# Optimization experiments

Hardware: AMD Instinct MI355X
Metric: run time of the kernel (lower is better)

## Reference

```python
import jax, jax.numpy as jnp
import numpy as np
import math

KV_STRIDE = 2
Q_STRIDE = 1
WAVE_LEN = 1000.0
POS_MAG = 1.0


def _pos_embed(h, w, h_kv, w_kv, q_stride, kv_stride, feat_dim):
    # Sinusoidal relative-position embeddings, matching get_position_embedding.
    h_idx = jnp.arange(h, dtype=jnp.float32) * q_stride
    w_idx = jnp.arange(w, dtype=jnp.float32) * q_stride
    h_kv_idx = jnp.arange(h_kv, dtype=jnp.float32) * kv_stride
    w_kv_idx = jnp.arange(w_kv, dtype=jnp.float32) * kv_stride
    h_diff = (h_idx[:, None] - h_kv_idx[None, :]) * POS_MAG  # (h, h_kv)
    w_diff = (w_idx[:, None] - w_kv_idx[None, :]) * POS_MAG  # (w, w_kv)
    feat_range = jnp.arange(feat_dim // 4, dtype=jnp.float32)
    dim_mat = WAVE_LEN ** (4.0 / feat_dim * feat_range)  # (feat_dim//4,)
    wd = w_diff[:, :, None] / dim_mat  # (w, w_kv, F)
    hd = h_diff[:, :, None] / dim_mat  # (h, h_kv, F)
    emb_x = jnp.concatenate([jnp.sin(wd), jnp.cos(wd)], axis=2)  # (w, w_kv, feat_dim//2)
    emb_y = jnp.concatenate([jnp.sin(hd), jnp.cos(hd)], axis=2)  # (h, h_kv, feat_dim//2)
    return emb_x, emb_y


def setup_inputs() -> dict:
    key = jax.random.key(0)
    ks = jax.random.split(key, 11)
    C = 288
    s = 1.0 / math.sqrt(C)
    return {
        'x_input': jax.random.normal(ks[0], (2, C, 64, 64), jnp.float32),
        'Wq': jax.random.normal(ks[1], (C, C), jnp.float32) * s,
        'Wk': jax.random.normal(ks[2], (C, C), jnp.float32) * s,
        'Wv': jax.random.normal(ks[3], (C, C), jnp.float32) * s,
        'Wx': jax.random.normal(ks[4], (C, C // 2), jnp.float32) * s,
        'Wy': jax.random.normal(ks[5], (C, C // 2), jnp.float32) * s,
        'Wproj': jax.random.normal(ks[6], (C, C), jnp.float32) * s,
        'bproj': jax.random.normal(ks[7], (C,), jnp.float32) * 0.02,
        'Wc': jax.random.normal(ks[8], (9, C), jnp.float32) * s,
        'bc': jax.random.normal(ks[9], (9,), jnp.float32) * 0.02,
        'gamma': jax.random.normal(ks[10], (1,), jnp.float32),
    }


def reference(x_input, Wq, Wk, Wv, Wx, Wy, Wproj, bproj, Wc, bc, gamma):
    M = Wc.shape[0]                       # num_mixtures
    n, C, h, w = x_input.shape
    d = Wq.shape[0] // M                  # qk_embed_dim (== v_dim)
    x_q = x_input                         # q_stride == 1
    x_kv = x_input[:, :, ::KV_STRIDE, ::KV_STRIDE]  # AvgPool2d(k=1, stride=2)
    h_kv, w_kv = x_kv.shape[2], x_kv.shape[3]

    # 1x1 convs as channel GEMMs
    q = jnp.einsum('nchw,oc->nohw', x_q, Wq).reshape(n, M, d, h * w)
    q = q.transpose(0, 1, 3, 2)                                    # (n,M,hw,d)
    k = jnp.einsum('nchw,oc->nohw', x_kv, Wk).reshape(n, M, d, h_kv * w_kv)

    emb_x, emb_y = _pos_embed(h, w, h_kv, w_kv, Q_STRIDE, KV_STRIDE, C)
    inv_sqrt2 = 1.0 / math.sqrt(2.0)
    pf_x = (emb_x @ Wx.T).reshape(w, w_kv, M, d).transpose(2, 0, 1, 3) * inv_sqrt2  # (M,w,w_kv,d)
    pf_y = (emb_y @ Wy.T).reshape(h, h_kv, M, d).transpose(2, 0, 1, 3) * inv_sqrt2  # (M,h,h_kv,d)

    energy = jnp.matmul(q, k).reshape(n, M, h, w, h_kv, w_kv)
    q5 = q.reshape(n, M, h, w, d)
    e_x = jnp.einsum('nmhwd,mwvd->nmhwv', q5, pf_x)  # (n,M,h,w,w_kv)
    e_y = jnp.einsum('nmhwd,mhud->nmhwu', q5, pf_y)  # (n,M,h,w,h_kv)
    energy = energy + e_x[:, :, :, :, None, :] + e_y[:, :, :, :, :, None]
    energy = energy.reshape(n, M, h * w, h_kv * w_kv)
    attn = jax.nn.softmax(energy, axis=3)

    # Learned per-mixture gating from mean query context
    context = q.transpose(0, 1, 3, 2).reshape(n, M * d, h * w).mean(axis=2)  # (n, M*d)
    mix_w = jax.nn.softmax(context @ Wc.T + bc, axis=1)                      # (n, M)
    attn = jnp.sum(attn * mix_w[:, :, None, None], axis=1)                   # (n,hw,hw_kv)

    v = jnp.einsum('nchw,oc->nohw', x_kv, Wv).reshape(n, M * d, h_kv * w_kv)
    v = v.transpose(0, 2, 1)                                                 # (n,hw_kv,M*d)
    out = jnp.matmul(attn, v).transpose(0, 2, 1).reshape(n, M * d, h, w)
    out = jnp.einsum('nchw,oc->nohw', out, Wproj) + bproj[None, :, None, None]
    return gamma[0] * out + x_input
```

## Files before the change

kernel.cpp:

```cpp
#include <hip/hip_runtime.h>
#include <math.h>

#define NB     2
#define CDIM   288
#define HW     4096
#define PKV    1024
#define MHEAD  9
#define DHEAD  32

typedef __attribute__((ext_vector_type(8))) short bf16x8;
typedef __attribute__((ext_vector_type(4))) float f32x4;

#if __has_builtin(__builtin_amdgcn_exp2f)
#define EXP2(x) __builtin_amdgcn_exp2f(x)
#else
#define EXP2(x) exp2f(x)
#endif

__device__ inline unsigned short f2bf(float x) {
    unsigned int u = __float_as_uint(x);
    u = (u + 0x7fffu + ((u >> 16) & 1u)) >> 16;
    return (unsigned short)u;
}


__global__ __launch_bounds__(256) void prep(const float* __restrict__ X,
        const float* __restrict__ Wq, const float* __restrict__ Wk,
        const float* __restrict__ Wv, const float* __restrict__ Wproj,
        const float* __restrict__ Wx, const float* __restrict__ Wy,
        unsigned short* __restrict__ XF, unsigned short* __restrict__ WFq,
        unsigned short* __restrict__ WFk, unsigned short* __restrict__ WFv,
        unsigned short* __restrict__ WFp, float* __restrict__ WTx,
        float* __restrict__ WTy, float* __restrict__ MX) {
    __shared__ float t32[32][133];
    __shared__ float t16[16][17];
    __shared__ float red[4];
    int b = blockIdx.x;
    int tid = threadIdx.x;
    if (b < 576) {
        int bx = b % 32, by = (b / 32) % 9, n = b / 288;
        int j0 = bx * 128, c0 = by * 32;
        int c = tid >> 3, f = tid & 7;
        const float* src = &X[((size_t)n * CDIM + c0 + c) * HW + j0];
#pragma unroll
        for (int l = 0; l < 4; ++l) {
            float4 v = *(const float4*)&src[(f + l * 8) * 4];
            *(float4*)&t32[c][(f + l * 8) * 4] = v;
        }
        __syncthreads();
        int cc = c0 >> 5;
#pragma unroll
        for (int l = 0; l < 4; ++l) {
            int g = l * 256 + tid;
            int s = g >> 7;
            int w = g & 127;
            int lane = w >> 1, e0 = (w & 1) * 4;
            int jl = s * 16 + (lane & 15);
            int cb = (lane >> 4) * 8 + e0;
            unsigned int w0 = f2bf(t32[cb + 0][jl]) | ((unsigned int)f2bf(t32[cb + 1][jl]) << 16);
            unsigned int w1 = f2bf(t32[cb + 2][jl]) | ((unsigned int)f2bf(t32[cb + 3][jl]) << 16);
            int jt = (j0 >> 4) + s;
            unsigned short* O = XF + (size_t)n * HW * CDIM + ((size_t)jt * 9 + cc) * 512 + lane * 8 + e0;
            uint2 pk = { w0, w1 };
            *(uint2*)O = pk;
        }
    } else if (b < 900) {
        int u = b - 576;
        int bx = u % 9, by = (u / 9) % 18, bz = u / 162;
        const float* W = bz ? Wy : Wx;
        float* WT      = bz ? WTy : WTx;
        int f0 = bx * 16, o0 = by * 16;
        int tx = tid & 15, ty = tid >> 4;
        t16[ty][tx] = W[(o0 + ty) * 144 + f0 + tx];
        __syncthreads();
        WT[(f0 + ty) * 288 + o0 + tx] = t16[tx][ty];
    } else if (b < 1062) {
        int t = b - 900;
        int sub = tid >> 6, lane = tid & 63;
        int ot = t / 9, cc = t % 9;
        const float* W = (sub == 0) ? Wq : (sub == 1) ? Wk : (sub == 2) ? Wv : Wproj;
        unsigned short* O = ((sub == 0) ? WFq : (sub == 1) ? WFk : (sub == 2) ? WFv : WFp)
                            + (size_t)t * 512;
        int o  = ot * 16 + (lane & 15);
        int c0 = cc * 32 + (lane >> 4) * 8;
        const float* src = W + (size_t)o * CDIM + c0;
        float4 f0 = *(const float4*)src, f1 = *(const float4*)(src + 4);
        unsigned int v0 = f2bf(f0.x) | ((unsigned int)f2bf(f0.y) << 16);
        unsigned int v1 = f2bf(f0.z) | ((unsigned int)f2bf(f0.w) << 16);
        unsigned int v2 = f2bf(f1.x) | ((unsigned int)f2bf(f1.y) << 16);
        unsigned int v3 = f2bf(f1.z) | ((unsigned int)f2bf(f1.w) << 16);
        uint4 pk = { v0, v1, v2, v3 };
        *(uint4*)(O + lane * 8) = pk;
    } else {
        int bid = b - 1062;
        const float* xr = X + (size_t)bid * HW;
        float s = 0.f;
        for (int j = tid; j < HW; j += 256) s += xr[j];
        for (int off = 32; off > 0; off >>= 1) s += __shfl_xor(s, off, 64);
        if ((tid & 63) == 0) red[tid >> 6] = s;
        __syncthreads();
        if (tid == 0) MX[bid] = (red[0] + red[1] + red[2] + red[3]) * (1.f / 4096.f);
    }
}

__global__ __launch_bounds__(256) void mid(
        const float* __restrict__ WTx, const float* __restrict__ WTy,
        unsigned short* __restrict__ FXb, unsigned short* __restrict__ FYb,
        const float* __restrict__ Wq, const float* __restrict__ MX,
        const float* __restrict__ Wc, const float* __restrict__ bc,
        float* __restrict__ MIXW,
        const unsigned short* __restrict__ WFq, const unsigned short* __restrict__ WFk,
        const unsigned short* __restrict__ WFv, const unsigned short* __restrict__ XF,
        unsigned short* __restrict__ Qf, unsigned short* __restrict__ KF,
        unsigned short* __restrict__ VF) {
    __shared__ float emb[144];
    __shared__ float ctx_s[NB * CDIM];
    __shared__ float lg[18];
    __shared__ __attribute__((aligned(16))) unsigned short tr[4][32][40];
    int b = blockIdx.x;
    int tid = threadIdx.x;

    if (b < 252) {
        int axis = b / 126;
        int dif  = b % 126;
        float diff = (float)(dif - 62);
        if (tid < 72) {
            float dm = expf(6.9077552789821368f * ((float)tid * (1.f / 72.f)));
            float t  = diff / dm;
            emb[tid]      = sinf(t);
            emb[72 + tid] = cosf(t);
        }
        __syncthreads();
        const float* WT = axis ? WTy : WTx;
        unsigned short* F = axis ? FYb : FXb;
        for (int o = tid; o < CDIM; o += 256) {
            float s = 0.f;
#pragma unroll 8
            for (int f = 0; f < 144; ++f) s += emb[f] * WT[f * 288 + o];
            int m = o >> 5, d = o & 31;
            F[(size_t)(m * 8 + (dif >> 4)) * 512 + ((dif & 15) + 16 * (d >> 3)) * 8 + (d & 7)]
                = f2bf(s * 0.70710678118654752f);
        }
    } else if (b == 252) {
        for (int idx = tid; idx < 1152; idx += 256) {
            int d = idx & 31, rr = (idx >> 5) & 1, mm = (idx >> 6) % 9, ax = idx / 576;
            int dif = 126 + rr;
            unsigned short* F = ax ? FYb : FXb;
            F[(size_t)(mm * 8 + 7) * 512 + ((dif & 15) + 16 * (d >> 3)) * 8 + (d & 7)] = 0;
        }
        for (int p = tid; p < NB * CDIM; p += 256) {
            int n = p / CDIM, o = p % CDIM;
            const float* wr = Wq + (size_t)o * CDIM;
            const float* mx = MX + n * CDIM;
            float s = 0.f;
            for (int c = 0; c < CDIM; c += 4) {
                float4 w4 = *(const float4*)&wr[c];
                float4 m4 = *(const float4*)&mx[c];
                s += w4.x * m4.x + w4.y * m4.y + w4.z * m4.z + w4.w * m4.w;
            }
            ctx_s[p] = s;
        }
        __syncthreads();
        if (tid < 18) {
            int n = tid / 9, j = tid % 9;
            float s = bc[j];
            for (int o = 0; o < CDIM; ++o) s += ctx_s[n * CDIM + o] * Wc[j * CDIM + o];
            lg[tid] = s;
        }
        __syncthreads();
        if (tid < 2) {
            float mx = -1e30f;
            for (int j = 0; j < 9; ++j) mx = fmaxf(mx, lg[tid * 9 + j]);
            float e[9], sm = 0.f;
            for (int j = 0; j < 9; ++j) { e[j] = __expf(lg[tid * 9 + j] - mx); sm += e[j]; }
            for (int j = 0; j < 9; ++j) MIXW[tid * 9 + j] = e[j] / sm;
        }
    } else {
        int bx = b - 253;
        int gx = bx % 40;
        int m  = (bx / 40) % 9;
        int n  = bx / 360;
        int wv = tid >> 6, lane = tid & 63;
        int lq = lane & 15, quad = lane >> 4;
        if (gx < 32) {
            int j0 = gx * 128;
            int jw = j0 + wv * 32;
            const unsigned short* Wb = WFq + ((size_t)(m * 2) * 9) * 512 + lane * 8;
            const unsigned short* Xb = XF + (size_t)n * HW * CDIM + ((size_t)(jw >> 4) * 9) * 512 + lane * 8;
            f32x4 acc[2][2] = {};
#pragma unroll
            for (int cc = 0; cc < 9; ++cc) {
                bf16x8 a0 = *(const bf16x8*)(Wb + (size_t)cc * 512);
                bf16x8 a1 = *(const bf16x8*)(Wb + (size_t)(9 + cc) * 512);
                bf16x8 b0 = *(const bf16x8*)(Xb + (size_t)cc * 512);
                bf16x8 b1 = *(const bf16x8*)(Xb + (size_t)(9 + cc) * 512);
                acc[0][0] = __builtin_amdgcn_mfma_f32_16x16x32_bf16(a0, b0, acc[0][0], 0, 0, 0);
                acc[0][1] = __builtin_amdgcn_mfma_f32_16x16x32_bf16(a0, b1, acc[0][1], 0, 0, 0);
                acc[1][0] = __builtin_amdgcn_mfma_f32_16x16x32_bf16(a1, b0, acc[1][0], 0, 0, 0);
                acc[1][1] = __builtin_amdgcn_mfma_f32_16x16x32_bf16(a1, b1, acc[1][1], 0, 0, 0);
            }
#pragma unroll
            for (int oi = 0; oi < 2; ++oi)
#pragma unroll
                for (int ji = 0; ji < 2; ++ji)
#pragma unroll
                    for (int r = 0; r < 4; ++r)
                        tr[wv][ji * 16 + lq][oi * 16 + quad * 4 + r]
                            = f2bf(1.4426950408889634f * acc[oi][ji][r]);
            int jl = lane & 31, half = lane >> 5;
            bf16x8 v0 = *(const bf16x8*)&tr[wv][jl][half * 16];
            bf16x8 v1 = *(const bf16x8*)&tr[wv][jl][half * 16 + 8];
            unsigned short* Qm = Qf + ((size_t)(n * MHEAD + m) * HW + jw + jl) * 32 + half * 16;
            *(bf16x8*)Qm = v0;
            *(bf16x8*)(Qm + 8) = v1;
        } else {
            int p0 = (gx - 32) * 128;
            int pw = p0 + wv * 32;
            const unsigned short* XFn = XF + (size_t)n * HW * CDIM;
            size_t bidx[2];
#pragma unroll
            for (int pi = 0; pi < 2; ++pi) {
                int p   = pw + pi * 16 + lq;
                int pos = ((p >> 5) << 7) + ((p & 31) << 1);
                bidx[pi] = ((size_t)(pos >> 4) * 9) * 512 + ((pos & 15) + 16 * quad) * 8;
            }
            const unsigned short* Wkb = WFk + ((size_t)(m * 2) * 9) * 512 + lane * 8;
            const unsigned short* Wvb = WFv + ((size_t)(m * 2) * 9) * 512 + lane * 8;
            f32x4 ak[2][2] = {}, av[2][2] = {};
#pragma unroll
            for (int cc = 0; cc < 9; ++cc) {
                bf16x8 a0k = *(const bf16x8*)(Wkb + (size_t)cc * 512);
                bf16x8 a1k = *(const bf16x8*)(Wkb + (size_t)(9 + cc) * 512);
                bf16x8 a0v = *(const bf16x8*)(Wvb + (size_t)cc * 512);
                bf16x8 a1v = *(const bf16x8*)(Wvb + (size_t)(9 + cc) * 512);
                bf16x8 b0  = *(const bf16x8*)(XFn + bidx[0] + (size_t)cc * 512);
                bf16x8 b1  = *(const bf16x8*)(XFn + bidx[1] + (size_t)cc * 512);
                ak[0][0] = __builtin_amdgcn_mfma_f32_16x16x32_bf16(a0k, b0, ak[0][0], 0, 0, 0);
                ak[0][1] = __builtin_amdgcn_mfma_f32_16x16x32_bf16(a0k, b1, ak[0][1], 0, 0, 0);
                ak[1][0] = __builtin_amdgcn_mfma_f32_16x16x32_bf16(a1k, b0, ak[1][0], 0, 0, 0);
                ak[1][1] = __builtin_amdgcn_mfma_f32_16x16x32_bf16(a1k, b1, ak[1][1], 0, 0, 0);
                av[0][0] = __builtin_amdgcn_mfma_f32_16x16x32_bf16(a0v, b0, av[0][0], 0, 0, 0);
                av[0][1] = __builtin_amdgcn_mfma_f32_16x16x32_bf16(a0v, b1, av[0][1], 0, 0, 0);
                av[1][0] = __builtin_amdgcn_mfma_f32_16x16x32_bf16(a1v, b0, av[1][0], 0, 0, 0);
                av[1][1] = __builtin_amdgcn_mfma_f32_16x16x32_bf16(a1v, b1, av[1][1], 0, 0, 0);
            }
#pragma unroll
            for (int oi = 0; oi < 2; ++oi)
#pragma unroll
                for (int pi = 0; pi < 2; ++pi)
#pragma unroll
                    for (int r = 0; r < 4; ++r)
                        tr[wv][pi * 16 + lq][oi * 16 + quad * 4 + r] = f2bf(ak[oi][pi][r]);
            unsigned short* KFm = KF + (size_t)(n * MHEAD + m) * (PKV * 32);
#pragma unroll
            for (int pi = 0; pi < 2; ++pi) {
                bf16x8 v = *(const bf16x8*)&tr[wv][pi * 16 + lq][quad * 8];
                *(bf16x8*)(KFm + (size_t)((pw >> 4) + pi) * 512 + lane * 8) = v;
            }
#pragma unroll
            for (int oi = 0; oi < 2; ++oi)
#pragma unroll
                for (int pi = 0; pi < 2; ++pi)
#pragma unroll
                    for (int r = 0; r < 4; ++r)
                        tr[wv][oi * 16 + quad * 4 + r][pi * 16 + lq] = f2bf(av[oi][pi][r]);
            unsigned short* VFn = VF + (size_t)n * CDIM * PKV;
#pragma unroll
            for (int oi = 0; oi < 2; ++oi) {
                bf16x8 v = *(const bf16x8*)&tr[wv][oi * 16 + lq][quad * 8];
                *(bf16x8*)(VFn + (size_t)((m * 2 + oi) * 32 + (pw >> 5)) * 512 + lane * 8) = v;
            }
        }
    }
}

__global__ __launch_bounds__(1024, 4) void attn_fused7(
        const unsigned short* __restrict__ Qf, const unsigned short* __restrict__ KF,
        const unsigned short* __restrict__ VF, const unsigned short* __restrict__ WFp,
        const unsigned short* __restrict__ FXb, const unsigned short* __restrict__ FYb,
        const float* __restrict__ MIXW, const float* __restrict__ bproj,
        const float* __restrict__ x, const float* __restrict__ gamma,
        float* __restrict__ OUT) {
    int n    = blockIdx.x >> 7;
    int i0   = (blockIdx.x & 127) * 32;
    int tid  = threadIdx.x;
    int wv   = tid >> 6;
    int ti   = wv >> 3;
    int w8   = wv & 7;
    int lane = tid & 63;
    int lq   = lane & 15;
    int quad = lane >> 4;
    int it0  = i0 + ti * 16;

    int bx_t = (it0 & 63) >> 4;
    int hh   = i0 >> 6;
    int by_t = hh >> 4;
    int dh   = hh & 15;

    __shared__ __attribute__((aligned(16))) unsigned short tr[32][1032];
    float (*Rx_s)[2][16][82] = reinterpret_cast<float (*)[2][16][82]>((char*)&tr[0][0]);
    float (*Ry_s)[2][16][82] = reinterpret_cast<float (*)[2][16][82]>((char*)&tr[0][0] + 20992);
    float (*ws_s)[2][16][8]  = reinterpret_cast<float (*)[2][16][8]>((char*)&tr[0][0] + 41984);
    unsigned short (*Mt)[296] = reinterpret_cast<unsigned short (*)[296]>(&tr[0][0]);

    float mixed[8][4];
#pragma unroll
    for (int t = 0; t < 8; ++t)
#pragma unroll
        for (int j = 0; j < 4; ++j) mixed[t][j] = 0.f;

    auto r_phase = [&](int mm, bf16x8 af) {
        int pp = mm & 1;
        if (w8 < 5) {
            bf16x8 bR = *(const bf16x8*)(FXb + (size_t)(mm * 8 + bx_t + w8) * 512 + lane * 8);
            f32x4 r = (f32x4){0.f, 0.f, 0.f, 0.f};
            r = __builtin_amdgcn_mfma_f32_16x16x32_bf16(af, bR, r, 0, 0, 0);
#pragma unroll
            for (int reg = 0; reg < 4; ++reg)
                Rx_s[pp][ti][quad * 4 + reg][w8 * 16 + lq] = r[reg];
        } else {
            bf16x8 bR = *(const bf16x8*)(FYb + (size_t)(mm * 8 + by_t + (w8 - 5)) * 512 + lane * 8);
            f32x4 r = (f32x4){0.f, 0.f, 0.f, 0.f};
            r = __builtin_amdgcn_mfma_f32_16x16x32_bf16(af, bR, r, 0, 0, 0);
#pragma unroll
            for (int reg = 0; reg < 4; ++reg)
                Ry_s[pp][ti][quad * 4 + reg][(w8 - 5) * 16 + lq] = r[reg];
        }
        if (w8 < 2) {
            bf16x8 bR = *(const bf16x8*)(FYb + (size_t)(mm * 8 + by_t + 3 + w8) * 512 + lane * 8);
            f32x4 r = (f32x4){0.f, 0.f, 0.f, 0.f};
            r = __builtin_amdgcn_mfma_f32_16x16x32_bf16(af, bR, r, 0, 0, 0);
#pragma unroll
            for (int reg = 0; reg < 4; ++reg)
                Ry_s[pp][ti][quad * 4 + reg][(3 + w8) * 16 + lq] = r[reg];
        }
    };

    bf16x8 af_cur = *(const bf16x8*)(Qf + (((size_t)n * MHEAD) * HW + it0 + lq) * 32 + quad * 8);
    r_phase(0, af_cur);
    __syncthreads();

#pragma unroll 1
    for (int m = 0; m < MHEAD; ++m) {
        const unsigned short* KmF = KF + (size_t)(n * MHEAD + m) * (PKV * 32);
        bf16x8 kf[8];
#pragma unroll
        for (int t = 0; t < 8; ++t)
            kf[t] = *(const bf16x8*)(KmF + (size_t)(w8 * 8 + t) * 512 + lane * 8);

        bf16x8 af_nxt = af_cur;
        __builtin_amdgcn_s_setprio(1);
        if (m + 1 < MHEAD) {
            af_nxt = *(const bf16x8*)(Qf + (((size_t)(n * MHEAD + m + 1)) * HW + it0 + lq) * 32 + quad * 8);
            r_phase(m + 1, af_nxt);
        }
        f32x4 acc[8];
#pragma unroll
        for (int t = 0; t < 8; ++t) {
            f32x4 z = (f32x4){0.f, 0.f, 0.f, 0.f};
            acc[t] = __builtin_amdgcn_mfma_f32_16x16x32_bf16(af_cur, kf[t], z, 0, 0, 0);
        }
        __builtin_amdgcn_s_setprio(0);

        int par = m & 1;
        float exA[4], exB[4];
#pragma unroll
        for (int j = 0; j < 4; ++j) {
            int q = quad * 4 + j;
            exA[j] = Rx_s[par][ti][q][q + 62 - 2 * lq];
            exB[j] = Rx_s[par][ti][q][q + 30 - 2 * lq];
        }
        float rs[4] = {0.f, 0.f, 0.f, 0.f};
#pragma unroll
        for (int tp = 0; tp < 4; ++tp) {
            int u = w8 * 4 + tp;
            float ey[4];
#pragma unroll
            for (int j = 0; j < 4; ++j) ey[j] = Ry_s[par][ti][quad * 4 + j][dh + 62 - 2 * u];
#pragma unroll
            for (int half = 0; half < 2; ++half) {
                int t = tp * 2 + half;
#pragma unroll
                for (int j = 0; j < 4; ++j) {
                    float e = EXP2(acc[t][j] + (half ? exB[j] : exA[j]) + ey[j]);
                    rs[j] += e;
                    acc[t][j] = e;
                }
            }
        }
#pragma unroll
        for (int j = 0; j < 4; ++j) {
            rs[j] += __shfl_xor(rs[j], 1, 64);
            rs[j] += __shfl_xor(rs[j], 2, 64);
            rs[j] += __shfl_xor(rs[j], 4, 64);
            rs[j] += __shfl_xor(rs[j], 8, 64);
        }
        if (lq == 0) {
#pragma unroll
            for (int j = 0; j < 4; ++j) ws_s[par][ti][quad * 4 + j][w8] = rs[j];
        }
        __syncthreads();

        {
            float wm = MIXW[n * MHEAD + m];
#pragma unroll
            for (int j = 0; j < 4; ++j) {
                int q = quad * 4 + j;
                float4 w0 = *(const float4*)&ws_s[par][ti][q][0];
                float4 w1 = *(const float4*)&ws_s[par][ti][q][4];
                float lt = (w0.x + w0.y) + (w0.z + w0.w) + (w1.x + w1.y) + (w1.z + w1.w);
                float fct = wm / lt;
#pragma unroll
                for (int t = 0; t < 8; ++t) mixed[t][j] += acc[t][j] * fct;
            }
        }
        __builtin_amdgcn_sched_barrier(0);
        af_cur = af_nxt;
    }

    __syncthreads();

#pragma unroll
    for (int t = 0; t < 8; ++t)
#pragma unroll
        for (int j = 0; j < 4; ++j)
            tr[ti * 16 + quad * 4 + j][w8 * 128 + t * 16 + lq] = f2bf(mixed[t][j]);
    __syncthreads();

    const unsigned short* VFn = VF + (size_t)n * CDIM * PKV;
    f32x4 accpv[2][2];
#pragma unroll
    for (int oi = 0; oi < 2; ++oi)
#pragma unroll
        for (int t2 = 0; t2 < 2; ++t2) accpv[oi][t2] = (f32x4){0.f, 0.f, 0.f, 0.f};
    bool has2 = (wv < 2);
#pragma unroll 4
    for (int pc = 0; pc < 32; ++pc) {
        bf16x8 pf0 = *(const bf16x8*)&tr[lq][pc * 32 + quad * 8];
        bf16x8 pf1 = *(const bf16x8*)&tr[16 + lq][pc * 32 + quad * 8];
        bf16x8 vf0 = *(const bf16x8*)(VFn + (size_t)(wv * 32 + pc) * 512 + lane * 8);
        accpv[0][0] = __builtin_amdgcn_mfma_f32_16x16x32_bf16(pf0, vf0, accpv[0][0], 0, 0, 0);
        accpv[0][1] = __builtin_amdgcn_mfma_f32_16x16x32_bf16(pf1, vf0, accpv[0][1], 0, 0, 0);
        if (has2) {
            bf16x8 vf1 = *(const bf16x8*)(VFn + (size_t)((wv + 16) * 32 + pc) * 512 + lane * 8);
            accpv[1][0] = __builtin_amdgcn_mfma_f32_16x16x32_bf16(pf0, vf1, accpv[1][0], 0, 0, 0);
            accpv[1][1] = __builtin_amdgcn_mfma_f32_16x16x32_bf16(pf1, vf1, accpv[1][1], 0, 0, 0);
        }
    }
    __syncthreads();

#pragma unroll
    for (int oi = 0; oi < 2; ++oi) {
        if (oi == 1 && !has2) continue;
        int ot = wv + oi * 16;
#pragma unroll
        for (int t2 = 0; t2 < 2; ++t2)
#pragma unroll
            for (int r = 0; r < 4; ++r)
                Mt[t2 * 16 + quad * 4 + r][ot * 16 + lq] = f2bf(accpv[oi][t2][r]);
    }
    __syncthreads();

    float g = gamma[0];
#pragma unroll
    for (int idx = 0; idx < 3; ++idx) {
        int ot = w8 + idx * 8;
        if (ot >= 18) continue;
        f32x4 acco = (f32x4){0.f, 0.f, 0.f, 0.f};
#pragma unroll
        for (int cc = 0; cc < 9; ++cc) {
            bf16x8 af = *(const bf16x8*)(WFp + (size_t)(ot * 9 + cc) * 512 + lane * 8);
            bf16x8 bfm = *(const bf16x8*)&Mt[ti * 16 + lq][cc * 32 + quad * 8];
            acco = __builtin_amdgcn_mfma_f32_16x16x32_bf16(af, bfm, acco, 0, 0, 0);
        }
#pragma unroll
        for (int r = 0; r < 4; ++r) {
            int o = ot * 16 + quad * 4 + r;
            size_t id = ((size_t)(n * CDIM) + o) * HW + it0 + lq;
            OUT[id] = g * (acco[r] + bproj[o]) + x[id];
        }
    }
}

extern "C" void kernel_launch(void* const* d_in, const int* in_sizes, int n_in,
                              void* d_out, int out_size, void* d_ws, size_t ws_size,
                              hipStream_t stream) {
    const float* x     = (const float*)d_in[0];
    const float* Wq    = (const float*)d_in[1];
    const float* Wk    = (const float*)d_in[2];
    const float* Wv    = (const float*)d_in[3];
    const float* Wx    = (const float*)d_in[4];
    const float* Wy    = (const float*)d_in[5];
    const float* Wproj = (const float*)d_in[6];
    const float* bproj = (const float*)d_in[7];
    const float* Wc    = (const float*)d_in[8];
    const float* bc    = (const float*)d_in[9];
    const float* gamma = (const float*)d_in[10];
    float* out = (float*)d_out;

    float* ws = (float*)d_ws;
    size_t off = 0;
    unsigned short* Qf  = (unsigned short*)(ws + off); off += (size_t)NB * MHEAD * HW * 32 / 2;
    unsigned short* KF  = (unsigned short*)(ws + off); off += (size_t)NB * MHEAD * PKV * 32 / 2;
    unsigned short* VF  = (unsigned short*)(ws + off); off += (size_t)NB * CDIM * PKV / 2;
    unsigned short* WFq = (unsigned short*)(ws + off); off += (size_t)CDIM * CDIM / 2;
    unsigned short* WFk = (unsigned short*)(ws + off); off += (size_t)CDIM * CDIM / 2;
    unsigned short* WFv = (unsigned short*)(ws + off); off += (size_t)CDIM * CDIM / 2;
    unsigned short* WFp = (unsigned short*)(ws + off); off += (size_t)CDIM * CDIM / 2;
    unsigned short* XF  = (unsigned short*)(ws + off); off += (size_t)NB * HW * CDIM / 2;
    float* WTx  = ws + off; off += 144 * 288;
    float* WTy  = ws + off; off += 144 * 288;
    unsigned short* FXb = (unsigned short*)(ws + off); off += (size_t)MHEAD * 8 * 512 / 2;
    unsigned short* FYb = (unsigned short*)(ws + off); off += (size_t)MHEAD * 8 * 512 / 2;
    float* MX   = ws + off; off += NB * CDIM;
    float* MIXW = ws + off; off += 32;

    prep<<<1638, 256, 0, stream>>>(x, Wq, Wk, Wv, Wproj, Wx, Wy,
                                   XF, WFq, WFk, WFv, WFp, WTx, WTy, MX);
    mid<<<973, 256, 0, stream>>>(WTx, WTy, FXb, FYb, Wq, MX, Wc, bc, MIXW,
                                 WFq, WFk, WFv, XF, Qf, KF, VF);
    attn_fused7<<<NB * HW / 32, 1024, 0, stream>>>(Qf, KF, VF, WFp, FXb, FYb, MIXW,
                                                   bproj, x, gamma, out);
}
```

Before: 174.3 us.

## Stage per-head K tiles into LDS with async loads and prefetch Q two heads ahead

```diff
diff --git a/kernel.cpp b/kernel.cpp
--- a/kernel.cpp
+++ b/kernel.cpp
@@ -11,6 +11,9 @@
 typedef __attribute__((ext_vector_type(8))) short bf16x8;
 typedef __attribute__((ext_vector_type(4))) float f32x4;
 
+typedef __attribute__((address_space(1))) const unsigned int gu32c;
+typedef __attribute__((address_space(3))) unsigned int lu32;
+
 #if __has_builtin(__builtin_amdgcn_exp2f)
 #define EXP2(x) __builtin_amdgcn_exp2f(x)
 #else
@@ -27,13 +30,10 @@
 __global__ __launch_bounds__(256) void prep(const float* __restrict__ X,
         const float* __restrict__ Wq, const float* __restrict__ Wk,
         const float* __restrict__ Wv, const float* __restrict__ Wproj,
-        const float* __restrict__ Wx, const float* __restrict__ Wy,
         unsigned short* __restrict__ XF, unsigned short* __restrict__ WFq,
         unsigned short* __restrict__ WFk, unsigned short* __restrict__ WFv,
-        unsigned short* __restrict__ WFp, float* __restrict__ WTx,
-        float* __restrict__ WTy, float* __restrict__ MX) {
+        unsigned short* __restrict__ WFp, float* __restrict__ MX) {
     __shared__ float t32[32][133];
-    __shared__ float t16[16][17];
     __shared__ float red[4];
     int b = blockIdx.x;
     int tid = threadIdx.x;
@@ -64,18 +64,8 @@
             uint2 pk = { w0, w1 };
             *(uint2*)O = pk;
         }
-    } else if (b < 900) {
-        int u = b - 576;
-        int bx = u % 9, by = (u / 9) % 18, bz = u / 162;
-        const float* W = bz ? Wy : Wx;
-        float* WT      = bz ? WTy : WTx;
-        int f0 = bx * 16, o0 = by * 16;
-        int tx = tid & 15, ty = tid >> 4;
-        t16[ty][tx] = W[(o0 + ty) * 144 + f0 + tx];
-        __syncthreads();
-        WT[(f0 + ty) * 288 + o0 + tx] = t16[tx][ty];
-    } else if (b < 1062) {
-        int t = b - 900;
+    } else if (b < 738) {
+        int t = b - 576;
         int sub = tid >> 6, lane = tid & 63;
         int ot = t / 9, cc = t % 9;
         const float* W = (sub == 0) ? Wq : (sub == 1) ? Wk : (sub == 2) ? Wv : Wproj;
@@ -92,7 +82,7 @@
         uint4 pk = { v0, v1, v2, v3 };
         *(uint4*)(O + lane * 8) = pk;
     } else {
-        int bid = b - 1062;
+        int bid = b - 738;
         const float* xr = X + (size_t)bid * HW;
         float s = 0.f;
         for (int j = tid; j < HW; j += 256) s += xr[j];
@@ -104,7 +94,7 @@
 }
 
 __global__ __launch_bounds__(256) void mid(
-        const float* __restrict__ WTx, const float* __restrict__ WTy,
+        const float* __restrict__ Wx, const float* __restrict__ Wy,
         unsigned short* __restrict__ FXb, unsigned short* __restrict__ FYb,
         const float* __restrict__ Wq, const float* __restrict__ MX,
         const float* __restrict__ Wc, const float* __restrict__ bc,
@@ -131,12 +121,17 @@
             emb[72 + tid] = cosf(t);
         }
         __syncthreads();
-        const float* WT = axis ? WTy : WTx;
+        const float* W = axis ? Wy : Wx;
         unsigned short* F = axis ? FYb : FXb;
         for (int o = tid; o < CDIM; o += 256) {
+            const float* wr = W + (size_t)o * 144;
             float s = 0.f;
-#pragma unroll 8
-            for (int f = 0; f < 144; ++f) s += emb[f] * WT[f * 288 + o];
+#pragma unroll 9
+            for (int f4 = 0; f4 < 36; ++f4) {
+                float4 w4 = *(const float4*)&wr[f4 * 4];
+                s += emb[f4 * 4 + 0] * w4.x + emb[f4 * 4 + 1] * w4.y
+                   + emb[f4 * 4 + 2] * w4.z + emb[f4 * 4 + 3] * w4.w;
+            }
             int m = o >> 5, d = o & 31;
             F[(size_t)(m * 8 + (dif >> 4)) * 512 + ((dif & 15) + 16 * (d >> 3)) * 8 + (d & 7)]
                 = f2bf(s * 0.70710678118654752f);
@@ -274,7 +269,7 @@
     }
 }
 
-__global__ __launch_bounds__(1024, 4) void attn_fused7(
+__global__ __launch_bounds__(1024, 4) void attn_fused8b(
         const unsigned short* __restrict__ Qf, const unsigned short* __restrict__ KF,
         const unsigned short* __restrict__ VF, const unsigned short* __restrict__ WFp,
         const unsigned short* __restrict__ FXb, const unsigned short* __restrict__ FYb,
@@ -298,6 +293,7 @@
     int dh   = hh & 15;
 
     __shared__ __attribute__((aligned(16))) unsigned short tr[32][1032];
+    __shared__ __attribute__((aligned(16))) unsigned short lds_kf[PKV * DHEAD];
     float (*Rx_s)[2][16][82] = reinterpret_cast<float (*)[2][16][82]>((char*)&tr[0][0]);
     float (*Ry_s)[2][16][82] = reinterpret_cast<float (*)[2][16][82]>((char*)&tr[0][0] + 20992);
     float (*ws_s)[2][16][8]  = reinterpret_cast<float (*)[2][16][8]>((char*)&tr[0][0] + 41984);
@@ -308,6 +304,16 @@
     for (int t = 0; t < 8; ++t)
 #pragma unroll
         for (int j = 0; j < 4; ++j) mixed[t][j] = 0.f;
+
+    auto stage_kf = [&](const unsigned short* KmX) {
+#pragma unroll
+        for (int L = 0; L < 4; ++L) {
+            int c = L * 16 + wv;
+            __builtin_amdgcn_global_load_lds(
+                (gu32c*)(KmX + (size_t)c * 512 + lane * 8),
+                (lu32*)(&lds_kf[c * 512]), 16, 0, 0);
+        }
+    };
 
     auto r_phase = [&](int mm, bf16x8 af) {
         int pp = mm & 1;
@@ -336,25 +342,36 @@
         }
     };
 
-    bf16x8 af_cur = *(const bf16x8*)(Qf + (((size_t)n * MHEAD) * HW + it0 + lq) * 32 + quad * 8);
+    auto load_af = [&](int mm) -> bf16x8 {
+        return *(const bf16x8*)(Qf + (((size_t)(n * MHEAD + mm)) * HW + it0 + lq) * 32 + quad * 8);
+    };
+
+    stage_kf(KF + (size_t)(n * MHEAD) * (PKV * 32));
+    bf16x8 af_cur = load_af(0);
+    bf16x8 af_nx1 = load_af(1);
     r_phase(0, af_cur);
+    asm volatile("s_waitcnt vmcnt(0)" ::: "memory");
     __syncthreads();
 
 #pragma unroll 1
     for (int m = 0; m < MHEAD; ++m) {
-        const unsigned short* KmF = KF + (size_t)(n * MHEAD + m) * (PKV * 32);
         bf16x8 kf[8];
 #pragma unroll
         for (int t = 0; t < 8; ++t)
-            kf[t] = *(const bf16x8*)(KmF + (size_t)(w8 * 8 + t) * 512 + lane * 8);
-
-        bf16x8 af_nxt = af_cur;
+            kf[t] = *(const bf16x8*)&lds_kf[(w8 * 8 + t) * 512 + lane * 8];
+        __syncthreads();
+
+        bf16x8 af_nx2 = af_nx1;
+        if (m + 1 < MHEAD) {
+            stage_kf(KF + (size_t)(n * MHEAD + m + 1) * (PKV * 32));
+            if (m + 2 < MHEAD) af_nx2 = load_af(m + 2);
+            __builtin_amdgcn_s_setprio(1);
+            r_phase(m + 1, af_nx1);
+            __builtin_amdgcn_s_setprio(0);
+        }
+
+        f32x4 acc[8];
         __builtin_amdgcn_s_setprio(1);
-        if (m + 1 < MHEAD) {
-            af_nxt = *(const bf16x8*)(Qf + (((size_t)(n * MHEAD + m + 1)) * HW + it0 + lq) * 32 + quad * 8);
-            r_phase(m + 1, af_nxt);
-        }
-        f32x4 acc[8];
 #pragma unroll
         for (int t = 0; t < 8; ++t) {
             f32x4 z = (f32x4){0.f, 0.f, 0.f, 0.f};
@@ -399,6 +416,7 @@
 #pragma unroll
             for (int j = 0; j < 4; ++j) ws_s[par][ti][quad * 4 + j][w8] = rs[j];
         }
+        asm volatile("s_waitcnt vmcnt(0)" ::: "memory");
         __syncthreads();
 
         {
@@ -415,7 +433,8 @@
             }
         }
         __builtin_amdgcn_sched_barrier(0);
-        af_cur = af_nxt;
+        af_cur = af_nx1;
+        af_nx1 = af_nx2;
     }
 
     __syncthreads();
@@ -508,17 +527,15 @@
     unsigned short* WFv = (unsigned short*)(ws + off); off += (size_t)CDIM * CDIM / 2;
     unsigned short* WFp = (unsigned short*)(ws + off); off += (size_t)CDIM * CDIM / 2;
     unsigned short* XF  = (unsigned short*)(ws + off); off += (size_t)NB * HW * CDIM / 2;
-    float* WTx  = ws + off; off += 144 * 288;
-    float* WTy  = ws + off; off += 144 * 288;
     unsigned short* FXb = (unsigned short*)(ws + off); off += (size_t)MHEAD * 8 * 512 / 2;
     unsigned short* FYb = (unsigned short*)(ws + off); off += (size_t)MHEAD * 8 * 512 / 2;
     float* MX   = ws + off; off += NB * CDIM;
     float* MIXW = ws + off; off += 32;
 
-    prep<<<1638, 256, 0, stream>>>(x, Wq, Wk, Wv, Wproj, Wx, Wy,
-                                   XF, WFq, WFk, WFv, WFp, WTx, WTy, MX);
-    mid<<<973, 256, 0, stream>>>(WTx, WTy, FXb, FYb, Wq, MX, Wc, bc, MIXW,
+    prep<<<1314, 256, 0, stream>>>(x, Wq, Wk, Wv, Wproj,
+                                   XF, WFq, WFk, WFv, WFp, MX);
+    mid<<<973, 256, 0, stream>>>(Wx, Wy, FXb, FYb, Wq, MX, Wc, bc, MIXW,
                                  WFq, WFk, WFv, XF, Qf, KF, VF);
-    attn_fused7<<<NB * HW / 32, 1024, 0, stream>>>(Qf, KF, VF, WFp, FXb, FYb, MIXW,
-                                                   bproj, x, gamma, out);
+    attn_fused8b<<<NB * HW / 32, 1024, 0, stream>>>(Qf, KF, VF, WFp, FXb, FYb, MIXW,
+                                                    bproj, x, gamma, out);
 }
```

New measurement: 179.8 us. +3.2%, slower.
